# Kernel tuning notes

Measured on AMD Instinct MI355X. Metric: run time of the kernel, lower is better.

The kernel has to match this reference:

```python
import jax, jax.numpy as jnp
import numpy as np

N = 8192        # nodes
D_IN = 512      # input features
H = 256         # hidden (GAT out_features)
D_OUT = 16      # output classes
K = 16          # num clusters/classes
LRELU_SLOPE = 0.2
MASK_FILL = -9e15
EDGE_P = 0.002  # sparsity of random adjacency


def setup_inputs() -> dict:
    key = jax.random.key(0)
    k1, k2, k3, k4, k5, k6 = jax.random.split(key, 6)
    x = jax.random.normal(k1, (N, D_IN), dtype=jnp.float32)
    # binary adjacency with self loops (module only tests adj > 0; support reused as propagation matrix)
    adj = (jax.random.uniform(k2, (N, N)) < EDGE_P).astype(jnp.float32)
    adj = jnp.maximum(adj, jnp.eye(N, dtype=jnp.float32))
    C_a = jax.random.normal(k3, (K, H), dtype=jnp.float32)
    # learned parameters (xavier-ish scale)
    W = jax.random.normal(k4, (D_IN, H), dtype=jnp.float32) * (1.414 * (2.0 / (D_IN + H)) ** 0.5)
    a = jax.random.normal(k5, (2 * H, 1), dtype=jnp.float32) * (1.414 * (2.0 / (2 * H + 1)) ** 0.5)
    W_gcn = jax.random.normal(k6, (H, D_OUT), dtype=jnp.float32)
    return {"x": x, "adj": adj, "C_a": C_a, "W": W, "a": a, "W_gcn": W_gcn}


def _clust_score(Z, C):
    # score[n,k] = exp(-||Z_n - C_k||) normalized over k (beta = 1)
    d = jnp.sqrt(((Z[:, None, :] - C[None, :, :]) ** 2).sum(-1))  # [N,K]
    s = jnp.exp(-d) + 1e-10
    return s / s.sum(axis=1, keepdims=True)


def reference(x, adj, C_a, W, a, W_gcn):
    h = W.shape[1]
    # --- GAT layer ---
    Wh = x @ W                                   # [N,H]
    Wh1 = Wh @ a[:h, :]                          # [N,1]
    Wh2 = Wh @ a[h:, :]                          # [N,1]
    e = jax.nn.leaky_relu(Wh1 + Wh2.T, LRELU_SLOPE)   # [N,N]
    att = jax.nn.softmax(jnp.where(adj > 0, e, MASK_FILL), axis=1)
    Z_0 = att @ Wh                               # h_prime, [N,H]
    gatoutput = jax.nn.elu(Z_0)
    # --- cluster score on detached Z_0 (update=False path) ---
    score = _clust_score(jax.lax.stop_gradient(Z_0), C_a)
    # --- GCN layer (B_1 = I, so Z_1 = F_1) ---
    F_1 = jax.nn.relu(adj @ (gatoutput @ W_gcn))  # [N,D_OUT]
    output = F_1
    Z_1 = F_1
    return (output, Z_1, Z_0, score)
```

## Files before the change

### kernel.cpp

```cpp
#include <hip/hip_runtime.h>
#include <hip/hip_bf16.h>

#define N_NODES 8192
#define D_IN    512
#define H       256
#define D_OUT   16
#define K_CL    16
#define MAXN    96

#define OUT_OFF 0
#define Z1_OFF  131072
#define Z0_OFF  262144
#define SC_OFF  2359296

typedef unsigned int   u32;
typedef unsigned short u16;

__device__ __forceinline__ float load_in(const void* p, int bf, size_t idx) {
    if (bf) { u32 w = ((const u16*)p)[idx]; return __uint_as_float(w << 16); }
    return ((const float*)p)[idx];
}
__device__ __forceinline__ void store_out(void* p, int bf, size_t idx, float v) {
    if (bf) ((__hip_bfloat16*)p)[idx] = __float2bfloat16(v);
    else    ((float*)p)[idx] = v;
}

__global__ void k_detect(const u32* __restrict__ adjw, int* __restrict__ flag) {
    int t = blockIdx.x * 256 + threadIdx.x;
    int hit = 0;
    #pragma unroll 4
    for (int i = 0; i < 64; i++)
        if (adjw[(size_t)t + (size_t)i * 16384] == 0x00003F80u) hit = 1;
    if (hit) atomicOr(flag, 1);
}

__global__ void k_prep_small(const void* av, const void* C_a, const void* Wgcn,
                             const int* __restrict__ flag,
                             float* a_f, float* Ca_f, float* Wg_f) {
    int bf = *flag;
    int i = blockIdx.x * 256 + threadIdx.x;
    if (i < 512)        a_f[i]         = load_in(av,   bf, i);
    else if (i < 4608)  Ca_f[i - 512]  = load_in(C_a,  bf, i - 512);
    else if (i < 8704)  Wg_f[i - 4608] = load_in(Wgcn, bf, i - 4608);
}

__global__ __launch_bounds__(256) void k_gemm_wh(
    const void* __restrict__ xraw, const void* __restrict__ wraw,
    const int* __restrict__ flag, float* __restrict__ Wh)
{
    int bf = *flag;
    __shared__ float xs[32][68];
    __shared__ float ws_[32][68];
    int tid = threadIdx.x;
    int bm = blockIdx.x >> 2, bn = blockIdx.x & 3;
    int m0 = bm * 64, n0 = bn * 64;
    int tx = tid & 15, ty = tid >> 4;
    float acc[4][4] = {};

    for (int k0 = 0; k0 < D_IN; k0 += 32) {
        {
            int r = tid >> 2, kq = (tid & 3) * 8;
            size_t base = (size_t)(m0 + r) * D_IN + k0 + kq;
            float v[8];
            if (bf) {
                uint4 raw = *(const uint4*)((const u16*)xraw + base);
                u32 rr[4] = {raw.x, raw.y, raw.z, raw.w};
                #pragma unroll
                for (int q = 0; q < 4; q++) {
                    v[2*q]   = __uint_as_float(rr[q] << 16);
                    v[2*q+1] = __uint_as_float(rr[q] & 0xFFFF0000u);
                }
            } else {
                float4 f0 = *(const float4*)((const float*)xraw + base);
                float4 f1 = *(const float4*)((const float*)xraw + base + 4);
                v[0]=f0.x; v[1]=f0.y; v[2]=f0.z; v[3]=f0.w;
                v[4]=f1.x; v[5]=f1.y; v[6]=f1.z; v[7]=f1.w;
            }
            #pragma unroll
            for (int u = 0; u < 8; u++) xs[kq + u][r] = v[u];
        }
        {
            int kk = tid >> 3, n8 = (tid & 7) * 8;
            size_t base = (size_t)(k0 + kk) * H + n0 + n8;
            if (bf) {
                uint4 raw = *(const uint4*)((const u16*)wraw + base);
                u32 rr[4] = {raw.x, raw.y, raw.z, raw.w};
                #pragma unroll
                for (int q = 0; q < 4; q++) {
                    ws_[kk][n8 + 2*q]   = __uint_as_float(rr[q] << 16);
                    ws_[kk][n8 + 2*q+1] = __uint_as_float(rr[q] & 0xFFFF0000u);
                }
            } else {
                float4 f0 = *(const float4*)((const float*)wraw + base);
                float4 f1 = *(const float4*)((const float*)wraw + base + 4);
                ws_[kk][n8+0]=f0.x; ws_[kk][n8+1]=f0.y; ws_[kk][n8+2]=f0.z; ws_[kk][n8+3]=f0.w;
                ws_[kk][n8+4]=f1.x; ws_[kk][n8+5]=f1.y; ws_[kk][n8+6]=f1.z; ws_[kk][n8+7]=f1.w;
            }
        }
        __syncthreads();
        #pragma unroll
        for (int kk = 0; kk < 32; kk++) {
            float4 a4 = *(const float4*)&xs[kk][ty * 4];
            float4 b4 = *(const float4*)&ws_[kk][tx * 4];
            float a[4] = {a4.x, a4.y, a4.z, a4.w};
            float b[4] = {b4.x, b4.y, b4.z, b4.w};
            #pragma unroll
            for (int i = 0; i < 4; i++)
                #pragma unroll
                for (int j = 0; j < 4; j++)
                    acc[i][j] += a[i] * b[j];
        }
        __syncthreads();
    }
    #pragma unroll
    for (int i = 0; i < 4; i++) {
        float4 o = {acc[i][0], acc[i][1], acc[i][2], acc[i][3]};
        *(float4*)&Wh[(size_t)(m0 + ty*4 + i) * H + n0 + tx*4] = o;
    }
}

__global__ __launch_bounds__(256) void k_wh12(
    const float* __restrict__ Wh, const float* __restrict__ a_f,
    float* __restrict__ Wh1, float* __restrict__ Wh2)
{
    int tid = threadIdx.x;
    int wave = tid >> 6, lane = tid & 63;
    int n = blockIdx.x * 4 + wave;
    float4 v  = *(const float4*)(Wh + (size_t)n * H + lane * 4);
    float4 a1 = *(const float4*)(a_f + lane * 4);
    float4 a2 = *(const float4*)(a_f + H + lane * 4);
    float s1 = v.x*a1.x + v.y*a1.y + v.z*a1.z + v.w*a1.w;
    float s2 = v.x*a2.x + v.y*a2.y + v.z*a2.z + v.w*a2.w;
    #pragma unroll
    for (int off = 32; off; off >>= 1) {
        s1 += __shfl_xor(s1, off);
        s2 += __shfl_xor(s2, off);
    }
    if (lane == 0) { Wh1[n] = s1; Wh2[n] = s2; }
}

__global__ __launch_bounds__(256) void k_gat_row(
    const void* __restrict__ adjraw, const int* __restrict__ flag,
    const float* __restrict__ Wh,
    const float* __restrict__ Wh1, const float* __restrict__ Wh2,
    const float* __restrict__ Ca_f, const float* __restrict__ Wg_f,
    float* __restrict__ Gf,
    int* __restrict__ nbr_cnt, u16* __restrict__ nbr_idx,
    void* __restrict__ dout)
{
    const int n = blockIdx.x;
    const int tid = threadIdx.x;
    const int bf = *flag;
    __shared__ int   s_cnt;
    __shared__ int   s_idx[MAXN];
    __shared__ float s_att[MAXN];
    __shared__ float s_z[H];
    __shared__ float s_g[H];
    __shared__ float s_red[256];
    __shared__ float s_sc[16];

    if (tid == 0) s_cnt = 0;
    __syncthreads();

    if (bf) {
        const u16* arow = (const u16*)adjraw + (size_t)n * N_NODES;
        #pragma unroll
        for (int it = 0; it < 4; it++) {
            int base = it * 2048 + tid * 8;
            uint4 raw = *(const uint4*)(arow + base);
            u32 rw[4] = {raw.x, raw.y, raw.z, raw.w};
            #pragma unroll
            for (int q = 0; q < 4; q++) {
                #pragma unroll
                for (int hh = 0; hh < 2; hh++) {
                    u32 u = (rw[q] >> (16 * hh)) & 0xFFFFu;
                    if (__uint_as_float(u << 16) > 0.f) {
                        int p = atomicAdd(&s_cnt, 1);
                        if (p < MAXN) s_idx[p] = base + q * 2 + hh;
                    }
                }
            }
        }
    } else {
        const float* arow = (const float*)adjraw + (size_t)n * N_NODES;
        #pragma unroll
        for (int it = 0; it < 8; it++) {
            int base = it * 1024 + tid * 4;
            float4 v = *(const float4*)(arow + base);
            float vv[4] = {v.x, v.y, v.z, v.w};
            #pragma unroll
            for (int q = 0; q < 4; q++) {
                if (vv[q] > 0.f) {
                    int p = atomicAdd(&s_cnt, 1);
                    if (p < MAXN) s_idx[p] = base + q;
                }
            }
        }
    }
    __syncthreads();
    const int cnt = min(s_cnt, MAXN);
    if (tid == 0) nbr_cnt[n] = cnt;
    if (tid < cnt) nbr_idx[(size_t)n * MAXN + tid] = (u16)s_idx[tid];

    float e = 0.f;
    if (tid < cnt) {
        float v = Wh1[n] + Wh2[s_idx[tid]];
        e = v > 0.f ? v : 0.2f * v;
    }
    s_red[tid] = (tid < cnt) ? e : -3e38f;
    __syncthreads();
    #pragma unroll
    for (int s = 128; s > 0; s >>= 1) {
        if (tid < s) s_red[tid] = fmaxf(s_red[tid], s_red[tid + s]);
        __syncthreads();
    }
    float m = s_red[0];
    __syncthreads();
    float wexp = (tid < cnt) ? expf(e - m) : 0.f;
    s_red[tid] = wexp;
    __syncthreads();
    #pragma unroll
    for (int s = 128; s > 0; s >>= 1) {
        if (tid < s) s_red[tid] += s_red[tid + s];
        __syncthreads();
    }
    float denom = s_red[0];
    if (tid < cnt) s_att[tid] = wexp / denom;
    __syncthreads();

    float acc = 0.f;
    for (int t = 0; t < cnt; t++)
        acc += s_att[t] * Wh[(size_t)s_idx[t] * H + tid];
    s_z[tid] = acc;
    store_out(dout, bf, (size_t)Z0_OFF + (size_t)n * H + tid, acc);
    s_g[tid] = acc > 0.f ? acc : expf(acc) - 1.f;
    __syncthreads();

    {
        int k = tid & 15, hb = (tid >> 4) * 16;
        float p = 0.f;
        #pragma unroll
        for (int i = 0; i < 16; i++) {
            float d = s_z[hb + i] - Ca_f[(size_t)k * H + hb + i];
            p += d * d;
        }
        s_red[tid] = p;
    }
    __syncthreads();
    if (tid < 16) {
        float d2 = 0.f;
        #pragma unroll
        for (int q = 0; q < 16; q++) d2 += s_red[q * 16 + tid];
        s_sc[tid] = expf(-sqrtf(d2)) + 1e-10f;
    }
    __syncthreads();
    if (tid < 16) {
        float tot = 0.f;
        #pragma unroll
        for (int q = 0; q < 16; q++) tot += s_sc[q];
        store_out(dout, bf, (size_t)SC_OFF + (size_t)n * K_CL + tid, s_sc[tid] / tot);
    }
    __syncthreads();

    {
        int o = tid & 15, hb = (tid >> 4) * 16;
        float p = 0.f;
        #pragma unroll
        for (int i = 0; i < 16; i++)
            p += s_g[hb + i] * Wg_f[(size_t)(hb + i) * D_OUT + o];
        s_red[tid] = p;
    }
    __syncthreads();
    if (tid < 16) {
        float g2 = 0.f;
        #pragma unroll
        for (int q = 0; q < 16; q++) g2 += s_red[q * 16 + tid];
        Gf[(size_t)n * D_OUT + tid] = g2;
    }
}

__global__ __launch_bounds__(256) void k_f1(
    const int* __restrict__ nbr_cnt, const u16* __restrict__ nbr_idx,
    const float* __restrict__ Gf, const int* __restrict__ flag,
    void* __restrict__ dout)
{
    int tid = threadIdx.x;
    int bf = *flag;
    int r = tid >> 4, o = tid & 15;
    int n = blockIdx.x * 16 + r;
    int cnt = nbr_cnt[n];
    const u16* idx = nbr_idx + (size_t)n * MAXN;
    float acc = 0.f;
    for (int t = 0; t < cnt; t++)
        acc += Gf[(size_t)idx[t] * D_OUT + o];
    acc = fmaxf(acc, 0.f);
    store_out(dout, bf, (size_t)OUT_OFF + (size_t)n * D_OUT + o, acc);
    store_out(dout, bf, (size_t)Z1_OFF  + (size_t)n * D_OUT + o, acc);
}

extern "C" void kernel_launch(void* const* d_in, const int* in_sizes, int n_in,
                              void* d_out, int out_size, void* d_ws, size_t ws_size,
                              hipStream_t stream) {
    const void* x    = d_in[0];
    const void* adj  = d_in[1];
    const void* C_a  = d_in[2];
    const void* W    = d_in[3];
    const void* av   = d_in[4];
    const void* Wgcn = d_in[5];

    char* wsp = (char*)d_ws;
    int*   flag = (int*)wsp;                   wsp += 256;
    float* Wh   = (float*)wsp;                 wsp += (size_t)N_NODES * H * 4;
    float* Wh1  = (float*)wsp;                 wsp += (size_t)N_NODES * 4;
    float* Wh2  = (float*)wsp;                 wsp += (size_t)N_NODES * 4;
    float* Gf   = (float*)wsp;                 wsp += (size_t)N_NODES * D_OUT * 4;
    int*   ncnt = (int*)wsp;                   wsp += (size_t)N_NODES * 4;
    u16*   nidx = (u16*)wsp;                   wsp += (size_t)N_NODES * MAXN * 2;
    float* a_f  = (float*)wsp;                 wsp += 2 * H * 4;
    float* Ca_f = (float*)wsp;                 wsp += (size_t)K_CL * H * 4;
    float* Wg_f = (float*)wsp;                 wsp += (size_t)H * D_OUT * 4;

    hipMemsetAsync(flag, 0, sizeof(int), stream);
    k_detect    <<<64, 256, 0, stream>>>((const u32*)adj, flag);
    k_prep_small<<<34, 256, 0, stream>>>(av, C_a, Wgcn, flag, a_f, Ca_f, Wg_f);
    k_gemm_wh   <<<512, 256, 0, stream>>>(x, W, flag, Wh);
    k_wh12      <<<N_NODES / 4, 256, 0, stream>>>(Wh, a_f, Wh1, Wh2);
    k_gat_row   <<<N_NODES, 256, 0, stream>>>(adj, flag, Wh, Wh1, Wh2, Ca_f, Wg_f,
                                              Gf, ncnt, nidx, d_out);
    k_f1        <<<N_NODES / 16, 256, 0, stream>>>(ncnt, nidx, Gf, flag, d_out);
}
```

Before: 452.9 us.

## Use bf16 MFMA for the Wh GEMM and single-wave softmax in GAT rows

Replaces the LDS-tiled fp32 SIMT GEMM for x@W with a per-wave 16x16 bf16 MFMA kernel. The prep kernel now also writes a transposed bf16 copy of W so B-fragments load contiguously. The GAT row softmax moves from two block-wide LDS tree reductions to a single wave using shuffle reductions, and one redundant barrier is removed. The fp32 fallback path becomes a naive per-thread loop with no data reuse, which is slow if inputs are fp32.

```diff
diff --git a/kernel.cpp b/kernel.cpp
--- a/kernel.cpp
+++ b/kernel.cpp
@@ -15,6 +15,8 @@
 
 typedef unsigned int   u32;
 typedef unsigned short u16;
+typedef short s16x8 __attribute__((ext_vector_type(8)));
+typedef float f32x4 __attribute__((ext_vector_type(4)));
 
 __device__ __forceinline__ float load_in(const void* p, int bf, size_t idx) {
     if (bf) { u32 w = ((const u16*)p)[idx]; return __uint_as_float(w << 16); }
@@ -34,88 +36,57 @@
     if (hit) atomicOr(flag, 1);
 }
 
-__global__ void k_prep_small(const void* av, const void* C_a, const void* Wgcn,
-                             const int* __restrict__ flag,
-                             float* a_f, float* Ca_f, float* Wg_f) {
+__global__ void k_prep(const void* av, const void* C_a, const void* Wgcn, const void* W,
+                       const int* __restrict__ flag,
+                       float* a_f, float* Ca_f, float* Wg_f, u16* Wt) {
     int bf = *flag;
     int i = blockIdx.x * 256 + threadIdx.x;
     if (i < 512)        a_f[i]         = load_in(av,   bf, i);
     else if (i < 4608)  Ca_f[i - 512]  = load_in(C_a,  bf, i - 512);
     else if (i < 8704)  Wg_f[i - 4608] = load_in(Wgcn, bf, i - 4608);
+    else if (i < 139776 && bf) {
+        int j = i - 8704;
+        int nn = j >> 9, kk = j & 511;
+        Wt[j] = ((const u16*)W)[(size_t)kk * H + nn];
+    }
 }
 
 __global__ __launch_bounds__(256) void k_gemm_wh(
     const void* __restrict__ xraw, const void* __restrict__ wraw,
-    const int* __restrict__ flag, float* __restrict__ Wh)
+    const u16* __restrict__ Wt, const int* __restrict__ flag,
+    float* __restrict__ Wh)
 {
     int bf = *flag;
-    __shared__ float xs[32][68];
-    __shared__ float ws_[32][68];
-    int tid = threadIdx.x;
-    int bm = blockIdx.x >> 2, bn = blockIdx.x & 3;
-    int m0 = bm * 64, n0 = bn * 64;
-    int tx = tid & 15, ty = tid >> 4;
-    float acc[4][4] = {};
-
-    for (int k0 = 0; k0 < D_IN; k0 += 32) {
-        {
-            int r = tid >> 2, kq = (tid & 3) * 8;
-            size_t base = (size_t)(m0 + r) * D_IN + k0 + kq;
-            float v[8];
-            if (bf) {
-                uint4 raw = *(const uint4*)((const u16*)xraw + base);
-                u32 rr[4] = {raw.x, raw.y, raw.z, raw.w};
-                #pragma unroll
-                for (int q = 0; q < 4; q++) {
-                    v[2*q]   = __uint_as_float(rr[q] << 16);
-                    v[2*q+1] = __uint_as_float(rr[q] & 0xFFFF0000u);
-                }
-            } else {
-                float4 f0 = *(const float4*)((const float*)xraw + base);
-                float4 f1 = *(const float4*)((const float*)xraw + base + 4);
-                v[0]=f0.x; v[1]=f0.y; v[2]=f0.z; v[3]=f0.w;
-                v[4]=f1.x; v[5]=f1.y; v[6]=f1.z; v[7]=f1.w;
-            }
-            #pragma unroll
-            for (int u = 0; u < 8; u++) xs[kq + u][r] = v[u];
-        }
-        {
-            int kk = tid >> 3, n8 = (tid & 7) * 8;
-            size_t base = (size_t)(k0 + kk) * H + n0 + n8;
-            if (bf) {
-                uint4 raw = *(const uint4*)((const u16*)wraw + base);
-                u32 rr[4] = {raw.x, raw.y, raw.z, raw.w};
-                #pragma unroll
-                for (int q = 0; q < 4; q++) {
-                    ws_[kk][n8 + 2*q]   = __uint_as_float(rr[q] << 16);
-                    ws_[kk][n8 + 2*q+1] = __uint_as_float(rr[q] & 0xFFFF0000u);
-                }
-            } else {
-                float4 f0 = *(const float4*)((const float*)wraw + base);
-                float4 f1 = *(const float4*)((const float*)wraw + base + 4);
-                ws_[kk][n8+0]=f0.x; ws_[kk][n8+1]=f0.y; ws_[kk][n8+2]=f0.z; ws_[kk][n8+3]=f0.w;
-                ws_[kk][n8+4]=f1.x; ws_[kk][n8+5]=f1.y; ws_[kk][n8+6]=f1.z; ws_[kk][n8+7]=f1.w;
-            }
-        }
-        __syncthreads();
-        #pragma unroll
-        for (int kk = 0; kk < 32; kk++) {
-            float4 a4 = *(const float4*)&xs[kk][ty * 4];
-            float4 b4 = *(const float4*)&ws_[kk][tx * 4];
-            float a[4] = {a4.x, a4.y, a4.z, a4.w};
-            float b[4] = {b4.x, b4.y, b4.z, b4.w};
-            #pragma unroll
-            for (int i = 0; i < 4; i++)
-                #pragma unroll
-                for (int j = 0; j < 4; j++)
-                    acc[i][j] += a[i] * b[j];
-        }
-        __syncthreads();
-    }
-    #pragma unroll
-    for (int i = 0; i < 4; i++) {
-        float4 o = {acc[i][0], acc[i][1], acc[i][2], acc[i][3]};
-        *(float4*)&Wh[(size_t)(m0 + ty*4 + i) * H + n0 + tx*4] = o;
+    int tid = threadIdx.x, wave = tid >> 6, lane = tid & 63;
+    int w = blockIdx.x * 4 + wave;
+    int mt = w >> 4, nt = w & 15;
+    int m0 = mt * 16, n0 = nt * 16;
+    int quad = lane >> 4, lr = lane & 15;
+
+    if (bf) {
+        const u16* xa = (const u16*)xraw + (size_t)(m0 + lr) * D_IN + quad * 8;
+        const u16* bb = Wt + (size_t)(n0 + lr) * D_IN + quad * 8;
+        f32x4 acc = {0.f, 0.f, 0.f, 0.f};
+        #pragma unroll
+        for (int k0 = 0; k0 < D_IN; k0 += 32) {
+            s16x8 a = *(const s16x8*)(xa + k0);
+            s16x8 b = *(const s16x8*)(bb + k0);
+            acc = __builtin_amdgcn_mfma_f32_16x16x32_bf16(a, b, acc, 0, 0, 0);
+        }
+        float* cp = Wh + (size_t)(m0 + quad * 4) * H + n0 + lr;
+        #pragma unroll
+        for (int i = 0; i < 4; i++) cp[(size_t)i * H] = acc[i];
+    } else {
+        const float* xa = (const float*)xraw + (size_t)(m0 + lr) * D_IN;
+        const float* wb = (const float*)wraw;
+        float c0 = 0.f, c1 = 0.f, c2 = 0.f, c3 = 0.f;
+        for (int k = 0; k < D_IN; k++) {
+            float a = xa[k];
+            const float* wr = wb + (size_t)k * H + n0 + quad * 4;
+            c0 += a * wr[0]; c1 += a * wr[1]; c2 += a * wr[2]; c3 += a * wr[3];
+        }
+        float* cp = Wh + (size_t)(m0 + lr) * H + n0 + quad * 4;
+        cp[0] = c0; cp[1] = c1; cp[2] = c2; cp[3] = c3;
     }
 }
 
@@ -150,6 +121,7 @@
 {
     const int n = blockIdx.x;
     const int tid = threadIdx.x;
+    const int wave = tid >> 6, lane = tid & 63;
     const int bf = *flag;
     __shared__ int   s_cnt;
     __shared__ int   s_idx[MAXN];
@@ -202,30 +174,24 @@
     if (tid == 0) nbr_cnt[n] = cnt;
     if (tid < cnt) nbr_idx[(size_t)n * MAXN + tid] = (u16)s_idx[tid];
 
-    float e = 0.f;
-    if (tid < cnt) {
-        float v = Wh1[n] + Wh2[s_idx[tid]];
-        e = v > 0.f ? v : 0.2f * v;
-    }
-    s_red[tid] = (tid < cnt) ? e : -3e38f;
-    __syncthreads();
-    #pragma unroll
-    for (int s = 128; s > 0; s >>= 1) {
-        if (tid < s) s_red[tid] = fmaxf(s_red[tid], s_red[tid + s]);
-        __syncthreads();
-    }
-    float m = s_red[0];
-    __syncthreads();
-    float wexp = (tid < cnt) ? expf(e - m) : 0.f;
-    s_red[tid] = wexp;
-    __syncthreads();
-    #pragma unroll
-    for (int s = 128; s > 0; s >>= 1) {
-        if (tid < s) s_red[tid] += s_red[tid + s];
-        __syncthreads();
-    }
-    float denom = s_red[0];
-    if (tid < cnt) s_att[tid] = wexp / denom;
+    if (wave == 0) {
+        int t1 = lane, t2 = 64 + lane;
+        float whn = Wh1[n];
+        float e1 = -3e38f, e2 = -3e38f;
+        if (t1 < cnt) { float v = whn + Wh2[s_idx[t1]]; e1 = v > 0.f ? v : 0.2f * v; }
+        if (t2 < cnt) { float v = whn + Wh2[s_idx[t2]]; e2 = v > 0.f ? v : 0.2f * v; }
+        float m = fmaxf(e1, e2);
+        #pragma unroll
+        for (int off = 32; off; off >>= 1) m = fmaxf(m, __shfl_xor(m, off));
+        float x1 = (t1 < cnt) ? expf(e1 - m) : 0.f;
+        float x2 = (t2 < cnt) ? expf(e2 - m) : 0.f;
+        float s = x1 + x2;
+        #pragma unroll
+        for (int off = 32; off; off >>= 1) s += __shfl_xor(s, off);
+        float inv = 1.f / s;
+        if (t1 < cnt) s_att[t1] = x1 * inv;
+        if (t2 < cnt) s_att[t2] = x2 * inv;
+    }
     __syncthreads();
 
     float acc = 0.f;
@@ -260,8 +226,6 @@
         for (int q = 0; q < 16; q++) tot += s_sc[q];
         store_out(dout, bf, (size_t)SC_OFF + (size_t)n * K_CL + tid, s_sc[tid] / tot);
     }
-    __syncthreads();
-
     {
         int o = tid & 15, hb = (tid >> 4) * 16;
         float p = 0.f;
@@ -319,13 +283,14 @@
     float* a_f  = (float*)wsp;                 wsp += 2 * H * 4;
     float* Ca_f = (float*)wsp;                 wsp += (size_t)K_CL * H * 4;
     float* Wg_f = (float*)wsp;                 wsp += (size_t)H * D_OUT * 4;
+    u16*   Wt   = (u16*)wsp;                   wsp += (size_t)H * D_IN * 2;
 
     hipMemsetAsync(flag, 0, sizeof(int), stream);
-    k_detect    <<<64, 256, 0, stream>>>((const u32*)adj, flag);
-    k_prep_small<<<34, 256, 0, stream>>>(av, C_a, Wgcn, flag, a_f, Ca_f, Wg_f);
-    k_gemm_wh   <<<512, 256, 0, stream>>>(x, W, flag, Wh);
-    k_wh12      <<<N_NODES / 4, 256, 0, stream>>>(Wh, a_f, Wh1, Wh2);
-    k_gat_row   <<<N_NODES, 256, 0, stream>>>(adj, flag, Wh, Wh1, Wh2, Ca_f, Wg_f,
-                                              Gf, ncnt, nidx, d_out);
-    k_f1        <<<N_NODES / 16, 256, 0, stream>>>(ncnt, nidx, Gf, flag, d_out);
-}
+    k_detect <<<64, 256, 0, stream>>>((const u32*)adj, flag);
+    k_prep   <<<546, 256, 0, stream>>>(av, C_a, Wgcn, W, flag, a_f, Ca_f, Wg_f, Wt);
+    k_gemm_wh<<<2048, 256, 0, stream>>>(x, W, Wt, flag, Wh);
+    k_wh12   <<<N_NODES / 4, 256, 0, stream>>>(Wh, a_f, Wh1, Wh2);
+    k_gat_row<<<N_NODES, 256, 0, stream>>>(adj, flag, Wh, Wh1, Wh2, Ca_f, Wg_f,
+                                           Gf, ncnt, nidx, d_out);
+    k_f1     <<<N_NODES / 16, 256, 0, stream>>>(ncnt, nidx, Gf, flag, d_out);
+}
```

Result: slower. 639.3 us (+41.2%).
